# Kernel optimization log

Measured on AMD Instinct MI355X. Metric: run time of the kernel, lower is better.

Reference implementation:

```python
import jax, jax.numpy as jnp
import numpy as np

N = 8192        # num_nodes
H = 128         # h_dim
E = 131072      # num edges (avg degree 16)
NREL = 90       # num relations
NB = 8          # num_bases (block-diagonal decomposition)
SI = H // NB    # block size 16


def setup_inputs() -> dict:
    key = jax.random.key(0)
    ks = jax.random.split(key, 24)
    sc = 0.01
    n = lambda k, shape, s=sc: jax.random.normal(k, shape, dtype=jnp.float32) * s
    return {
        'node_ids': jnp.arange(N, dtype=jnp.int32),
        'src': jax.random.randint(ks[0], (E,), 0, N, dtype=jnp.int32),
        'dst': jax.random.randint(ks[1], (E,), 0, N, dtype=jnp.int32),
        'etypes': jax.random.randint(ks[2], (E,), 0, NREL, dtype=jnp.int32),
        'norm': jax.random.uniform(ks[3], (E, 1), dtype=jnp.float32),
        'eps': jax.random.normal(ks[4], (N, H), dtype=jnp.float32),
        # input embedding layer
        'embedding': n(ks[5], (N, H)),
        # RelGraphConv layer 0 ('bdd'): per-relation block-diag weights, self-loop, bias
        'W0': n(ks[6], (NREL, NB, SI, SI)),
        'loop0': n(ks[7], (H, H)),
        'b0': jnp.zeros((H,), jnp.float32),
        # RelGraphConv layer 1
        'W1': n(ks[8], (NREL, NB, SI, SI)),
        'loop1': n(ks[9], (H, H)),
        'b1': jnp.zeros((H,), jnp.float32),
        # z_layer: Linear(H, 2H)  (weights stored as (in, out))
        'Wz': n(ks[10], (H, 2 * H)),
        'bz': jnp.zeros((2 * H,), jnp.float32),
        # inter_layer (UpdateLayer): Linear(H, H) + h_bias
        'Wi': n(ks[11], (H, H)),
        'bi': jnp.zeros((H,), jnp.float32),
        'hbi': jnp.zeros((H,), jnp.float32),
        # output_layer (second UpdateLayer)
        'Wo': n(ks[12], (H, H)),
        'bo': jnp.zeros((H,), jnp.float32),
        'hbo': jnp.zeros((H,), jnp.float32),
    }


def _rgcn_bdd(h, W, loop_w, bias, src, dst, etypes, norm, act):
    # gather src features, split into NB blocks of size SI
    x = h[src].reshape(-1, NB, SI)                       # [E, NB, SI]
    Wg = W[etypes]                                       # [E, NB, SI, SI] per-edge relation block weights
    msg = jnp.einsum('ebi,ebio->ebo', x, Wg).reshape(-1, H) * norm  # [E, H]
    agg = jax.ops.segment_sum(msg, dst, num_segments=N)  # scatter-add to dst
    out = agg + bias + h @ loop_w                        # self-loop + bias
    return act(out) if act is not None else out


def reference(node_ids, src, dst, etypes, norm, eps, embedding,
              W0, loop0, b0, W1, loop1, b1,
              Wz, bz, Wi, bi, hbi, Wo, bo, hbo):
    # input layer: embedding lookup; saved as input_embed
    x0 = embedding[node_ids]                             # [N, H]
    h = _rgcn_bdd(x0, W0, loop0, b0, src, dst, etypes, norm, jax.nn.relu)
    h = _rgcn_bdd(h, W1, loop1, b1, src, dst, etypes, norm, None)
    # VAE head: z ~ N(mean, exp(log_std))
    zml = h @ Wz + bz                                    # [N, 2H]
    z_mean, z_log_std = jnp.split(zml, 2, axis=-1)
    z = z_mean + jnp.exp(z_log_std) * eps                # reparameterized sample
    # decode 1: outer-product reconstruction + fused update
    R = z @ z.T                                          # [N, N]
    h = R @ (z @ Wi + bi) + R @ x0 + hbi
    # decode 2
    R2 = h @ h.T                                         # [N, N]
    out = R2 @ (h @ Wo + bo) + R2 @ x0 + hbo
    return out
```

## Files before the change

kernel.cpp:

```cpp
#include <hip/hip_runtime.h>
#include <hip/hip_bf16.h>
#include <math.h>

#define Hdim 128
#define NBq 8
#define SIq 16

typedef __attribute__((ext_vector_type(8))) short short8x;
typedef __attribute__((ext_vector_type(4))) float f32x4;

__device__ inline unsigned short f2b(float f) {
  unsigned int u = __float_as_uint(f);
  return (unsigned short)((u + 0x7fffu + ((u >> 16) & 1u)) >> 16);
}
__device__ inline unsigned int pack2(float lo, float hi) {
  return (unsigned int)f2b(lo) | ((unsigned int)f2b(hi) << 16);
}

__global__ __launch_bounds__(256) void k_pre(
    const float* __restrict__ emb, const int* __restrict__ ids, float* __restrict__ x0,
    const float* __restrict__ W0, unsigned short* __restrict__ Wt0,
    const float* __restrict__ W1, unsigned short* __restrict__ Wt1, int w0elems,
    const float* __restrict__ l0, const float* __restrict__ l1,
    const float* __restrict__ Wi, const float* __restrict__ Wo, const float* __restrict__ Wz,
    unsigned short* __restrict__ l0t, unsigned short* __restrict__ l1t,
    unsigned short* __restrict__ Wit, unsigned short* __restrict__ Wot,
    unsigned short* __restrict__ Wzt,
    const int* __restrict__ dst, int* __restrict__ cnt, int E,
    int b1, int b2, int b3) {
  int bx = blockIdx.x, t = threadIdx.x;
  if (bx < b1) {
    int idx = bx * 256 + t;
    int n = idx >> 5, c4 = idx & 31;
    int s = ids[n];
    ((float4*)x0)[(size_t)n * 32 + c4] = ((const float4*)emb)[(size_t)s * 32 + c4];
  } else if (bx < b2) {
    int idx = (bx - b1) * 256 + t;
    const float* W = (idx < w0elems) ? W0 : W1;
    unsigned short* Wt = (idx < w0elems) ? Wt0 : Wt1;
    int local = (idx < w0elems) ? idx : idx - w0elems;
    int rb = local >> 8, io = local & 255;
    int i = io >> 4, o = io & 15;
    Wt[(size_t)rb * 256 + o * 16 + i] = f2b(W[(size_t)rb * 256 + i * 16 + o]);
  } else if (bx < b3) {
    int idx = (bx - b2) * 256 + t;
    if (idx < 65536) {
      int w = idx >> 14, local = idx & 16383;
      const float* in = (w == 0) ? l0 : (w == 1) ? l1 : (w == 2) ? Wi : Wo;
      unsigned short* out = (w == 0) ? l0t : (w == 1) ? l1t : (w == 2) ? Wit : Wot;
      int n = local >> 7, k = local & 127;
      out[local] = f2b(in[k * 128 + n]);
    } else {
      int local = idx - 65536;
      int n = local >> 7, k = local & 127;
      Wzt[local] = f2b(Wz[k * 256 + n]);
    }
  } else {
    int e = (bx - b3) * 256 + t;
    if (e < E) atomicAdd(&cnt[dst[e]], 1);
  }
}

__global__ __launch_bounds__(1024) void k_scan(const int* __restrict__ cnt,
                                               int* __restrict__ off,
                                               int* __restrict__ cur, int N, int E) {
  __shared__ int part[1024];
  int t = threadIdx.x;
  int ipt = N / 1024;
  int base = t * ipt;
  int loc[8];
  int s = 0;
  for (int i = 0; i < ipt; ++i) { loc[i] = s; s += cnt[base + i]; }
  part[t] = s;
  __syncthreads();
  for (int d = 1; d < 1024; d <<= 1) {
    int v = part[t];
    int add = (t >= d) ? part[t - d] : 0;
    __syncthreads();
    part[t] = v + add;
    __syncthreads();
  }
  int pre = (t == 0) ? 0 : part[t - 1];
  for (int i = 0; i < ipt; ++i) {
    int o = pre + loc[i];
    off[base + i] = o;
    cur[base + i] = o;
  }
  if (t == 0) off[N] = E;
}

__global__ void k_scatter(const int* __restrict__ src, const int* __restrict__ dst,
                          const int* __restrict__ et, const float* __restrict__ norm,
                          int* __restrict__ cur, int* __restrict__ psrc,
                          int* __restrict__ pet, float* __restrict__ pnorm, int E) {
  int e = blockIdx.x * blockDim.x + threadIdx.x;
  if (e >= E) return;
  int p = atomicAdd(&cur[dst[e]], 1);
  psrc[p] = src[e];
  pet[p]  = et[e];
  pnorm[p] = norm[e];
}

#define BF_LO(u) __uint_as_float((u) << 16)
#define BF_HI(u) __uint_as_float((u) & 0xffff0000u)
__global__ __launch_bounds__(128) void k_edge4(
    const float* __restrict__ h, const unsigned short* __restrict__ Wt,
    const int* __restrict__ off, const int* __restrict__ psrc,
    const int* __restrict__ pet, const float* __restrict__ pnorm,
    float* __restrict__ agg) {
  int n = blockIdx.x;
  int f = threadIdx.x;
  int b = f >> 4, o = f & 15;
  int j0 = off[n], j1 = off[n + 1];
  __shared__ float xs[8][Hdim];
  float acc = 0.f;
  for (int j = j0; j < j1; j += 8) {
    int m = min(8, j1 - j);
    for (int q = 0; q < m; ++q)
      xs[q][f] = h[(size_t)psrc[j + q] * Hdim + f];
    __syncthreads();
    for (int q = 0; q < m; ++q) {
      int r = pet[j + q];
      float nv = pnorm[j + q];
      const uint4* wp = (const uint4*)(Wt + ((size_t)r * NBq + b) * 256 + o * 16);
      uint4 wa = wp[0], wb = wp[1];
      const float4* xp = (const float4*)(&xs[q][b * SIq]);
      float4 x0 = xp[0], x1 = xp[1], x2 = xp[2], x3 = xp[3];
      float a = x0.x*BF_LO(wa.x) + x0.y*BF_HI(wa.x) + x0.z*BF_LO(wa.y) + x0.w*BF_HI(wa.y)
              + x1.x*BF_LO(wa.z) + x1.y*BF_HI(wa.z) + x1.z*BF_LO(wa.w) + x1.w*BF_HI(wa.w)
              + x2.x*BF_LO(wb.x) + x2.y*BF_HI(wb.x) + x2.z*BF_LO(wb.y) + x2.w*BF_HI(wb.y)
              + x3.x*BF_LO(wb.z) + x3.y*BF_HI(wb.z) + x3.z*BF_LO(wb.w) + x3.w*BF_HI(wb.w);
      acc = fmaf(a, nv, acc);
    }
    __syncthreads();
  }
  agg[(size_t)n * Hdim + f] = acc;
}

__global__ __launch_bounds__(256) void k_bgemm(
    const float* __restrict__ A, const unsigned short* __restrict__ Bt,
    const float* __restrict__ Gsrc, float* __restrict__ C,
    const float* __restrict__ addm, const float* __restrict__ bias,
    int M, int Nc, int relu, float* __restrict__ gzero) {
  __shared__ unsigned short Al[32][136];
  __shared__ unsigned short Bl[64][136];
  int t = threadIdx.x;
  int bm = blockIdx.x * 32, bn = blockIdx.y * 64;
  if (gzero && blockIdx.x == 0 && blockIdx.y == 0) {
#pragma unroll
    for (int i = 0; i < 16; ++i)
      ((float4*)gzero)[t + 256 * i] = make_float4(0.f, 0.f, 0.f, 0.f);
  }
  {
    int r = t >> 3, c0 = (t & 7) << 4;
    const float4* ap = (const float4*)(A + (size_t)(bm + r) * Hdim + c0);
    float4 a0 = ap[0], a1 = ap[1], a2 = ap[2], a3 = ap[3];
    uint4 p0 = { pack2(a0.x, a0.y), pack2(a0.z, a0.w), pack2(a1.x, a1.y), pack2(a1.z, a1.w) };
    uint4 p1 = { pack2(a2.x, a2.y), pack2(a2.z, a2.w), pack2(a3.x, a3.y), pack2(a3.z, a3.w) };
    *(uint4*)&Al[r][c0]     = p0;
    *(uint4*)&Al[r][c0 + 8] = p1;
  }
  if (Bt) {
    int n = t >> 2, k0 = (t & 3) << 5;
    const uint4* bp = (const uint4*)(Bt + (size_t)(bn + n) * Hdim + k0);
    uint4 b0 = bp[0], b1 = bp[1], b2 = bp[2], b3 = bp[3];
    *(uint4*)&Bl[n][k0]      = b0;
    *(uint4*)&Bl[n][k0 + 8]  = b1;
    *(uint4*)&Bl[n][k0 + 16] = b2;
    *(uint4*)&Bl[n][k0 + 24] = b3;
  } else {
    int n = t & 63, kb = (t >> 6) << 5;
    for (int i = 0; i < 32; ++i) {
      int k = kb + i;
      Bl[n][k] = f2b(Gsrc[(size_t)k * 128 + bn + n]);
    }
  }
  __syncthreads();
  int wv = t >> 6, ln = t & 63;
  int mt = wv & 1;
  int nt0 = (wv >> 1) << 1;
  int lm = ln & 15, lk = ln >> 4;
  f32x4 acc0 = {0.f, 0.f, 0.f, 0.f}, acc1 = {0.f, 0.f, 0.f, 0.f};
#pragma unroll
  for (int ks = 0; ks < 4; ++ks) {
    short8x af = *(const short8x*)&Al[mt * 16 + lm][ks * 32 + lk * 8];
    short8x bf0 = *(const short8x*)&Bl[nt0 * 16 + lm][ks * 32 + lk * 8];
    short8x bf1 = *(const short8x*)&Bl[(nt0 + 1) * 16 + lm][ks * 32 + lk * 8];
    acc0 = __builtin_amdgcn_mfma_f32_16x16x32_bf16(af, bf0, acc0, 0, 0, 0);
    acc1 = __builtin_amdgcn_mfma_f32_16x16x32_bf16(af, bf1, acc1, 0, 0, 0);
  }
  int gcol0 = bn + nt0 * 16 + lm;
  int gcol1 = gcol0 + 16;
  float b0v = bias ? bias[gcol0] : 0.f;
  float b1v = bias ? bias[gcol1] : 0.f;
#pragma unroll
  for (int reg = 0; reg < 4; ++reg) {
    int grow = bm + mt * 16 + lk * 4 + reg;
    size_t o0 = (size_t)grow * Nc + gcol0;
    size_t o1 = (size_t)grow * Nc + gcol1;
    float v0 = acc0[reg] + b0v;
    float v1 = acc1[reg] + b1v;
    if (addm) { v0 += addm[o0]; v1 += addm[o1]; }
    if (relu) { v0 = fmaxf(v0, 0.f); v1 = fmaxf(v1, 0.f); }
    C[o0] = v0;
    C[o1] = v1;
  }
}

__global__ __launch_bounds__(256) void k_bgemm_z(
    const float* __restrict__ A, const unsigned short* __restrict__ Wzt,
    const float* __restrict__ bz, const float* __restrict__ eps,
    float* __restrict__ Z, int M) {
  __shared__ unsigned short Al[32][136];
  __shared__ unsigned short Bm[64][136];
  __shared__ unsigned short Bl[64][136];
  int t = threadIdx.x;
  int bm = blockIdx.x * 32, bn = blockIdx.y * 64;
  {
    int r = t >> 3, c0 = (t & 7) << 4;
    const float4* ap = (const float4*)(A + (size_t)(bm + r) * Hdim + c0);
    float4 a0 = ap[0], a1 = ap[1], a2 = ap[2], a3 = ap[3];
    uint4 p0 = { pack2(a0.x, a0.y), pack2(a0.z, a0.w), pack2(a1.x, a1.y), pack2(a1.z, a1.w) };
    uint4 p1 = { pack2(a2.x, a2.y), pack2(a2.z, a2.w), pack2(a3.x, a3.y), pack2(a3.z, a3.w) };
    *(uint4*)&Al[r][c0]     = p0;
    *(uint4*)&Al[r][c0 + 8] = p1;
  }
  {
    int n = t >> 2, k0 = (t & 3) << 5;
    const uint4* mp = (const uint4*)(Wzt + (size_t)(bn + n) * Hdim + k0);
    const uint4* lp = (const uint4*)(Wzt + (size_t)(bn + 128 + n) * Hdim + k0);
    uint4 m0 = mp[0], m1 = mp[1], m2 = mp[2], m3 = mp[3];
    uint4 l0 = lp[0], l1 = lp[1], l2 = lp[2], l3 = lp[3];
    *(uint4*)&Bm[n][k0]      = m0; *(uint4*)&Bm[n][k0 + 8]  = m1;
    *(uint4*)&Bm[n][k0 + 16] = m2; *(uint4*)&Bm[n][k0 + 24] = m3;
    *(uint4*)&Bl[n][k0]      = l0; *(uint4*)&Bl[n][k0 + 8]  = l1;
    *(uint4*)&Bl[n][k0 + 16] = l2; *(uint4*)&Bl[n][k0 + 24] = l3;
  }
  __syncthreads();
  int wv = t >> 6, ln = t & 63;
  int mt = wv & 1;
  int nt0 = (wv >> 1) << 1;
  int lm = ln & 15, lk = ln >> 4;
  f32x4 am0 = {0,0,0,0}, am1 = {0,0,0,0}, al0 = {0,0,0,0}, al1 = {0,0,0,0};
#pragma unroll
  for (int ks = 0; ks < 4; ++ks) {
    short8x af = *(const short8x*)&Al[mt * 16 + lm][ks * 32 + lk * 8];
    short8x bm0 = *(const short8x*)&Bm[nt0 * 16 + lm][ks * 32 + lk * 8];
    short8x bm1 = *(const short8x*)&Bm[(nt0 + 1) * 16 + lm][ks * 32 + lk * 8];
    short8x bl0 = *(const short8x*)&Bl[nt0 * 16 + lm][ks * 32 + lk * 8];
    short8x bl1 = *(const short8x*)&Bl[(nt0 + 1) * 16 + lm][ks * 32 + lk * 8];
    am0 = __builtin_amdgcn_mfma_f32_16x16x32_bf16(af, bm0, am0, 0, 0, 0);
    am1 = __builtin_amdgcn_mfma_f32_16x16x32_bf16(af, bm1, am1, 0, 0, 0);
    al0 = __builtin_amdgcn_mfma_f32_16x16x32_bf16(af, bl0, al0, 0, 0, 0);
    al1 = __builtin_amdgcn_mfma_f32_16x16x32_bf16(af, bl1, al1, 0, 0, 0);
  }
  int gcol0 = bn + nt0 * 16 + lm;
  int gcol1 = gcol0 + 16;
  float bm0v = bz[gcol0], bm1v = bz[gcol1];
  float bl0v = bz[128 + gcol0], bl1v = bz[128 + gcol1];
#pragma unroll
  for (int reg = 0; reg < 4; ++reg) {
    int grow = bm + mt * 16 + lk * 4 + reg;
    size_t o0 = (size_t)grow * Hdim + gcol0;
    size_t o1 = (size_t)grow * Hdim + gcol1;
    Z[o0] = am0[reg] + bm0v + expf(al0[reg] + bl0v) * eps[o0];
    Z[o1] = am1[reg] + bm1v + expf(al1[reg] + bl1v) * eps[o1];
  }
}

__global__ __launch_bounds__(256) void k_xty(const float* __restrict__ X,
                                             const float* __restrict__ Y,
                                             float* __restrict__ G, int N) {
  __shared__ float xs[8][64];
  __shared__ float ys[8][64];
  int t  = threadIdx.x;
  int tx = t & 15, ty = t >> 4;
  int qr = blockIdx.y >> 1, qc = blockIdx.y & 1;
  int KC = N / gridDim.x;
  int k0 = blockIdx.x * KC;
  int m  = t >> 7, li = t & 127;
  int lr = li >> 4, lc = (li & 15) << 2;
  const float* S = m ? Y : X;
  int coff = (m ? qc : qr) * 64;
  float acc[4][4] = {};
  for (int kb = 0; kb < KC; kb += 8) {
    float4 v = *(const float4*)(S + (size_t)(k0 + kb + lr) * Hdim + coff + lc);
    __syncthreads();
    if (m) *(float4*)&ys[lr][lc] = v; else *(float4*)&xs[lr][lc] = v;
    __syncthreads();
#pragma unroll
    for (int kk = 0; kk < 8; ++kk) {
      float4 xv = *(const float4*)&xs[kk][ty << 2];
      float4 yv = *(const float4*)&ys[kk][tx << 2];
      acc[0][0] += xv.x * yv.x; acc[0][1] += xv.x * yv.y; acc[0][2] += xv.x * yv.z; acc[0][3] += xv.x * yv.w;
      acc[1][0] += xv.y * yv.x; acc[1][1] += xv.y * yv.y; acc[1][2] += xv.y * yv.z; acc[1][3] += xv.y * yv.w;
      acc[2][0] += xv.z * yv.x; acc[2][1] += xv.z * yv.y; acc[2][2] += xv.z * yv.z; acc[2][3] += xv.z * yv.w;
      acc[3][0] += xv.w * yv.x; acc[3][1] += xv.w * yv.y; acc[3][2] += xv.w * yv.z; acc[3][3] += xv.w * yv.w;
    }
  }
  int grow = qr * 64 + (ty << 2);
  int gcol = qc * 64 + (tx << 2);
#pragma unroll
  for (int r = 0; r < 4; ++r)
#pragma unroll
    for (int c = 0; c < 4; ++c)
      atomicAdd(&G[(size_t)(grow + r) * Hdim + gcol + c], acc[r][c]);
}

extern "C" void kernel_launch(void* const* d_in, const int* in_sizes, int n_in,
                              void* d_out, int out_size, void* d_ws, size_t ws_size,
                              hipStream_t stream) {
  const int*   node_ids = (const int*)d_in[0];
  const int*   src      = (const int*)d_in[1];
  const int*   dst      = (const int*)d_in[2];
  const int*   et       = (const int*)d_in[3];
  const float* norm     = (const float*)d_in[4];
  const float* eps      = (const float*)d_in[5];
  const float* emb      = (const float*)d_in[6];
  const float* W0       = (const float*)d_in[7];
  const float* loop0    = (const float*)d_in[8];
  const float* b0       = (const float*)d_in[9];
  const float* W1       = (const float*)d_in[10];
  const float* loop1    = (const float*)d_in[11];
  const float* b1       = (const float*)d_in[12];
  const float* Wz       = (const float*)d_in[13];
  const float* bz       = (const float*)d_in[14];
  const float* Wi       = (const float*)d_in[15];
  const float* bi       = (const float*)d_in[16];
  const float* hbi      = (const float*)d_in[17];
  const float* Wo       = (const float*)d_in[18];
  const float* bo       = (const float*)d_in[19];
  const float* hbo      = (const float*)d_in[20];
  float* out = (float*)d_out;

  const int N  = in_sizes[0];
  const int E  = in_sizes[1];
  const int RB = in_sizes[7] / (SIq * SIq);

  char* ws = (char*)d_ws;
  const size_t MB = 1u << 20;
  const size_t KB = 1u << 10;
  float* X0   = (float*)(ws + 0 * MB);
  float* B1p  = (float*)(ws + 4 * MB);
  float* B2p  = (float*)(ws + 8 * MB);
  float* AGG  = (float*)(ws + 12 * MB);
  float* B3p  = (float*)(ws + 16 * MB);
  float* G    = (float*)(ws + 20 * MB);
  int*   offp = (int*)(ws + 20 * MB + 256 * KB);
  int*   curp = (int*)(ws + 20 * MB + 512 * KB);
  int*   cntp = (int*)(ws + 20 * MB + 768 * KB);
  int*   psrc = (int*)(ws + 21 * MB);
  int*   pet  = (int*)(ws + 21 * MB + 512 * KB);
  float* pnrm = (float*)(ws + 22 * MB);
  unsigned short* Wt0 = (unsigned short*)(ws + 22 * MB + 512 * KB);
  unsigned short* Wt1 = (unsigned short*)(ws + 23 * MB);
  unsigned short* l0t = (unsigned short*)(ws + 24 * MB);
  unsigned short* l1t = (unsigned short*)(ws + 24 * MB + 64 * KB);
  unsigned short* Wit = (unsigned short*)(ws + 24 * MB + 128 * KB);
  unsigned short* Wot = (unsigned short*)(ws + 24 * MB + 192 * KB);
  unsigned short* Wzt = (unsigned short*)(ws + 24 * MB + 256 * KB);

  dim3 blk(256);

  const int w0elems = RB * 256;
  const int gB   = (N * 32) / 256;
  const int wtbB = (2 * w0elems + 255) / 256;
  const int wttB = 98304 / 256;
  const int histB = (E + 255) / 256;
  const int b1s = gB, b2s = gB + wtbB, b3s = gB + wtbB + wttB;
  hipMemsetAsync(cntp, 0, (size_t)N * sizeof(int), stream);
  k_pre<<<dim3(b3s + histB), blk, 0, stream>>>(
      emb, node_ids, X0, W0, Wt0, W1, Wt1, w0elems,
      loop0, loop1, Wi, Wo, Wz, l0t, l1t, Wit, Wot, Wzt,
      dst, cntp, E, b1s, b2s, b3s);
  k_scan<<<dim3(1), dim3(1024), 0, stream>>>(cntp, offp, curp, N, E);
  k_scatter<<<dim3((E + 255) / 256), blk, 0, stream>>>(src, dst, et, norm, curp,
                                                       psrc, pet, pnrm, E);

  k_edge4<<<dim3(N), dim3(128), 0, stream>>>(X0, Wt0, offp, psrc, pet, pnrm, AGG);
  k_bgemm<<<dim3(N / 32, 2), blk, 0, stream>>>(X0, l0t, nullptr, B1p, AGG, b0, N, Hdim, 1, nullptr);
  k_edge4<<<dim3(N), dim3(128), 0, stream>>>(B1p, Wt1, offp, psrc, pet, pnrm, AGG);
  k_bgemm<<<dim3(N / 32, 2), blk, 0, stream>>>(B1p, l1t, nullptr, B2p, AGG, b1, N, Hdim, 0, nullptr);
  k_bgemm_z<<<dim3(N / 32, 2), blk, 0, stream>>>(B2p, Wzt, bz, eps, B1p, N);
  k_bgemm<<<dim3(N / 32, 2), blk, 0, stream>>>(B1p, Wit, nullptr, B3p, X0, bi, N, Hdim, 0, G);
  k_xty<<<dim3(32, 4), blk, 0, stream>>>(B1p, B3p, G, N);
  k_bgemm<<<dim3(N / 32, 2), blk, 0, stream>>>(B1p, nullptr, G, B2p, nullptr, hbi, N, Hdim, 0, nullptr);
  k_bgemm<<<dim3(N / 32, 2), blk, 0, stream>>>(B2p, Wot, nullptr, B3p, X0, bo, N, Hdim, 0, G);
  k_xty<<<dim3(32, 4), blk, 0, stream>>>(B2p, B3p, G, N);
  k_bgemm<<<dim3(N / 32, 2), blk, 0, stream>>>(B2p, nullptr, G, out, nullptr, hbo, N, Hdim, 0, nullptr);
}
```

Baseline: 296.1 us.

## Fuse tail GEMM chain into one cooperative kernel and pair nodes in edge kernel

Merges the eight tail launches (self-loop GEMM, z head, update GEMMs, X^T Y reductions) into one cooperative persistent kernel of 512 blocks, with grid-wide syncs replacing kernel boundaries. This is meant to remove launch and drain overhead between small dependent kernels. The edge aggregation kernel now handles two destination nodes per 256-thread block. Both halves loop to the longer node's chunk count, so the shorter half sits idle on those iterations. The cooperative launch needs all 512 blocks resident, and each grid sync has its own cost.

```diff
diff --git a/kernel.cpp b/kernel.cpp
--- a/kernel.cpp
+++ b/kernel.cpp
@@ -1,10 +1,13 @@
 #include <hip/hip_runtime.h>
 #include <hip/hip_bf16.h>
+#include <hip/hip_cooperative_groups.h>
 #include <math.h>
 
 #define Hdim 128
 #define NBq 8
 #define SIq 16
+
+namespace cg = cooperative_groups;
 
 typedef __attribute__((ext_vector_type(8))) short short8x;
 typedef __attribute__((ext_vector_type(4))) float f32x4;
@@ -103,28 +106,35 @@
 
 #define BF_LO(u) __uint_as_float((u) << 16)
 #define BF_HI(u) __uint_as_float((u) & 0xffff0000u)
-__global__ __launch_bounds__(128) void k_edge4(
+__global__ __launch_bounds__(256) void k_edge7(
     const float* __restrict__ h, const unsigned short* __restrict__ Wt,
     const int* __restrict__ off, const int* __restrict__ psrc,
     const int* __restrict__ pet, const float* __restrict__ pnorm,
     float* __restrict__ agg) {
-  int n = blockIdx.x;
-  int f = threadIdx.x;
+  int t = threadIdx.x;
+  int half = t >> 7;
+  int f = t & 127;
   int b = f >> 4, o = f & 15;
-  int j0 = off[n], j1 = off[n + 1];
-  __shared__ float xs[8][Hdim];
+  int nb = blockIdx.x * 2;
+  int c0 = off[nb], c1 = off[nb + 1], c2 = off[nb + 2];
+  int n  = nb + half;
+  int j0 = half ? c1 : c0;
+  int j1 = half ? c2 : c1;
+  int chunks = (max(c1 - c0, c2 - c1) + 7) >> 3;
+  __shared__ float xs[2][8][Hdim];
   float acc = 0.f;
-  for (int j = j0; j < j1; j += 8) {
+  for (int cb = 0; cb < chunks; ++cb) {
+    int j = j0 + cb * 8;
     int m = min(8, j1 - j);
     for (int q = 0; q < m; ++q)
-      xs[q][f] = h[(size_t)psrc[j + q] * Hdim + f];
+      xs[half][q][f] = h[(size_t)psrc[j + q] * Hdim + f];
     __syncthreads();
     for (int q = 0; q < m; ++q) {
       int r = pet[j + q];
       float nv = pnorm[j + q];
       const uint4* wp = (const uint4*)(Wt + ((size_t)r * NBq + b) * 256 + o * 16);
       uint4 wa = wp[0], wb = wp[1];
-      const float4* xp = (const float4*)(&xs[q][b * SIq]);
+      const float4* xp = (const float4*)(&xs[half][q][b * SIq]);
       float4 x0 = xp[0], x1 = xp[1], x2 = xp[2], x3 = xp[3];
       float a = x0.x*BF_LO(wa.x) + x0.y*BF_HI(wa.x) + x0.z*BF_LO(wa.y) + x0.w*BF_HI(wa.y)
               + x1.x*BF_LO(wa.z) + x1.y*BF_HI(wa.z) + x1.z*BF_LO(wa.w) + x1.w*BF_HI(wa.w)
@@ -137,16 +147,16 @@
   agg[(size_t)n * Hdim + f] = acc;
 }
 
-__global__ __launch_bounds__(256) void k_bgemm(
-    const float* __restrict__ A, const unsigned short* __restrict__ Bt,
-    const float* __restrict__ Gsrc, float* __restrict__ C,
-    const float* __restrict__ addm, const float* __restrict__ bias,
-    int M, int Nc, int relu, float* __restrict__ gzero) {
-  __shared__ unsigned short Al[32][136];
-  __shared__ unsigned short Bl[64][136];
+__device__ void d_bgemm(char* sm, const float* __restrict__ A,
+                        const unsigned short* __restrict__ Bt,
+                        const float* __restrict__ Gsrc, float* __restrict__ C,
+                        const float* __restrict__ addm, const float* __restrict__ bias,
+                        int relu, float* __restrict__ gzero, int tile) {
+  unsigned short (*Al)[136] = (unsigned short(*)[136])sm;
+  unsigned short (*Bl)[136] = (unsigned short(*)[136])(sm + 32 * 136 * 2);
   int t = threadIdx.x;
-  int bm = blockIdx.x * 32, bn = blockIdx.y * 64;
-  if (gzero && blockIdx.x == 0 && blockIdx.y == 0) {
+  int bm = (tile & 255) * 32, bn = (tile >> 8) * 64;
+  if (gzero && tile == 0) {
 #pragma unroll
     for (int i = 0; i < 16; ++i)
       ((float4*)gzero)[t + 256 * i] = make_float4(0.f, 0.f, 0.f, 0.f);
@@ -196,8 +206,8 @@
 #pragma unroll
   for (int reg = 0; reg < 4; ++reg) {
     int grow = bm + mt * 16 + lk * 4 + reg;
-    size_t o0 = (size_t)grow * Nc + gcol0;
-    size_t o1 = (size_t)grow * Nc + gcol1;
+    size_t o0 = (size_t)grow * Hdim + gcol0;
+    size_t o1 = (size_t)grow * Hdim + gcol1;
     float v0 = acc0[reg] + b0v;
     float v1 = acc1[reg] + b1v;
     if (addm) { v0 += addm[o0]; v1 += addm[o1]; }
@@ -207,15 +217,25 @@
   }
 }
 
-__global__ __launch_bounds__(256) void k_bgemm_z(
-    const float* __restrict__ A, const unsigned short* __restrict__ Wzt,
-    const float* __restrict__ bz, const float* __restrict__ eps,
-    float* __restrict__ Z, int M) {
-  __shared__ unsigned short Al[32][136];
-  __shared__ unsigned short Bm[64][136];
-  __shared__ unsigned short Bl[64][136];
+__global__ __launch_bounds__(256) void k_bgemm(
+    const float* __restrict__ A, const unsigned short* __restrict__ Bt,
+    const float* __restrict__ Gsrc, float* __restrict__ C,
+    const float* __restrict__ addm, const float* __restrict__ bias,
+    int relu, float* __restrict__ gzero) {
+  __shared__ char sm[26112];
+  d_bgemm(sm, A, Bt, Gsrc, C, addm, bias, relu, gzero,
+          blockIdx.x + (blockIdx.y << 8));
+}
+
+__device__ void d_bgemm_z(char* sm, const float* __restrict__ A,
+                          const unsigned short* __restrict__ Wzt,
+                          const float* __restrict__ bz, const float* __restrict__ eps,
+                          float* __restrict__ Z, int tile) {
+  unsigned short (*Al)[136] = (unsigned short(*)[136])sm;
+  unsigned short (*Bm)[136] = (unsigned short(*)[136])(sm + 8704);
+  unsigned short (*Bl)[136] = (unsigned short(*)[136])(sm + 8704 + 17408);
   int t = threadIdx.x;
-  int bm = blockIdx.x * 32, bn = blockIdx.y * 64;
+  int bm = (tile & 255) * 32, bn = (tile >> 8) * 64;
   {
     int r = t >> 3, c0 = (t & 7) << 4;
     const float4* ap = (const float4*)(A + (size_t)(bm + r) * Hdim + c0);
@@ -268,16 +288,16 @@
   }
 }
 
-__global__ __launch_bounds__(256) void k_xty(const float* __restrict__ X,
-                                             const float* __restrict__ Y,
-                                             float* __restrict__ G, int N) {
-  __shared__ float xs[8][64];
-  __shared__ float ys[8][64];
+__device__ void d_xty(char* sm, const float* __restrict__ X, const float* __restrict__ Y,
+                      float* __restrict__ G, int N, int tile) {
+  float (*xs)[64] = (float(*)[64])sm;
+  float (*ys)[64] = (float(*)[64])(sm + 2048);
   int t  = threadIdx.x;
   int tx = t & 15, ty = t >> 4;
-  int qr = blockIdx.y >> 1, qc = blockIdx.y & 1;
-  int KC = N / gridDim.x;
-  int k0 = blockIdx.x * KC;
+  int quad = tile >> 5;
+  int qr = quad >> 1, qc = quad & 1;
+  int KC = N / 32;
+  int k0 = (tile & 31) * KC;
   int m  = t >> 7, li = t & 127;
   int lr = li >> 4, lc = (li & 15) << 2;
   const float* S = m ? Y : X;
@@ -305,6 +325,32 @@
 #pragma unroll
     for (int c = 0; c < 4; ++c)
       atomicAdd(&G[(size_t)(grow + r) * Hdim + gcol + c], acc[r][c]);
+}
+
+__global__ __launch_bounds__(256, 1) void k_tail(
+    float* B1p, float* B2p, float* B3p, const float* X0, const float* AGG, float* G,
+    const unsigned short* l1t, const unsigned short* Wit, const unsigned short* Wot,
+    const unsigned short* Wzt, const float* b1, const float* bz, const float* eps,
+    const float* bi, const float* hbi, const float* bo, const float* hbo,
+    float* out, int N) {
+  __shared__ char sm[43520];
+  cg::grid_group g = cg::this_grid();
+  int tile = blockIdx.x;
+  d_bgemm(sm, B1p, l1t, nullptr, B2p, AGG, b1, 0, nullptr, tile);
+  g.sync();
+  d_bgemm_z(sm, B2p, Wzt, bz, eps, B1p, tile);
+  g.sync();
+  d_bgemm(sm, B1p, Wit, nullptr, B3p, X0, bi, 0, G, tile);
+  g.sync();
+  if (tile < 128) d_xty(sm, B1p, B3p, G, N, tile);
+  g.sync();
+  d_bgemm(sm, B1p, nullptr, G, B2p, nullptr, hbi, 0, nullptr, tile);
+  g.sync();
+  d_bgemm(sm, B2p, Wot, nullptr, B3p, X0, bo, 0, G, tile);
+  g.sync();
+  if (tile < 128) d_xty(sm, B2p, B3p, G, N, tile);
+  g.sync();
+  d_bgemm(sm, B2p, nullptr, G, out, nullptr, hbo, 0, nullptr, tile);
 }
 
 extern "C" void kernel_launch(void* const* d_in, const int* in_sizes, int n_in,
@@ -377,15 +423,16 @@
   k_scatter<<<dim3((E + 255) / 256), blk, 0, stream>>>(src, dst, et, norm, curp,
                                                        psrc, pet, pnrm, E);
 
-  k_edge4<<<dim3(N), dim3(128), 0, stream>>>(X0, Wt0, offp, psrc, pet, pnrm, AGG);
-  k_bgemm<<<dim3(N / 32, 2), blk, 0, stream>>>(X0, l0t, nullptr, B1p, AGG, b0, N, Hdim, 1, nullptr);
-  k_edge4<<<dim3(N), dim3(128), 0, stream>>>(B1p, Wt1, offp, psrc, pet, pnrm, AGG);
-  k_bgemm<<<dim3(N / 32, 2), blk, 0, stream>>>(B1p, l1t, nullptr, B2p, AGG, b1, N, Hdim, 0, nullptr);
-  k_bgemm_z<<<dim3(N / 32, 2), blk, 0, stream>>>(B2p, Wzt, bz, eps, B1p, N);
-  k_bgemm<<<dim3(N / 32, 2), blk, 0, stream>>>(B1p, Wit, nullptr, B3p, X0, bi, N, Hdim, 0, G);
-  k_xty<<<dim3(32, 4), blk, 0, stream>>>(B1p, B3p, G, N);
-  k_bgemm<<<dim3(N / 32, 2), blk, 0, stream>>>(B1p, nullptr, G, B2p, nullptr, hbi, N, Hdim, 0, nullptr);
-  k_bgemm<<<dim3(N / 32, 2), blk, 0, stream>>>(B2p, Wot, nullptr, B3p, X0, bo, N, Hdim, 0, G);
-  k_xty<<<dim3(32, 4), blk, 0, stream>>>(B2p, B3p, G, N);
-  k_bgemm<<<dim3(N / 32, 2), blk, 0, stream>>>(B2p, nullptr, G, out, nullptr, hbo, N, Hdim, 0, nullptr);
-}
+  k_edge7<<<dim3(N / 2), blk, 0, stream>>>(X0, Wt0, offp, psrc, pet, pnrm, AGG);
+  k_bgemm<<<dim3(256, 2), blk, 0, stream>>>(X0, l0t, nullptr, B1p, AGG, b0, 1, nullptr);
+  k_edge7<<<dim3(N / 2), blk, 0, stream>>>(B1p, Wt1, offp, psrc, pet, pnrm, AGG);
+  {
+    void* targs[] = {
+      (void*)&B1p, (void*)&B2p, (void*)&B3p, (void*)&X0, (void*)&AGG, (void*)&G,
+      (void*)&l1t, (void*)&Wit, (void*)&Wot, (void*)&Wzt,
+      (void*)&b1, (void*)&bz, (void*)&eps, (void*)&bi, (void*)&hbi,
+      (void*)&bo, (void*)&hbo, (void*)&out, (void*)&N
+    };
+    hipLaunchCooperativeKernel((const void*)k_tail, dim3(512), blk, targs, 0, stream);
+  }
+}
```

New measurement: 736.4 us. 149% more time.
